# Performance work log

Measured on AMD Instinct MI355X. Metric: run time of the kernel, lower is better.

## Reference

```python
import jax, jax.numpy as jnp
import numpy as np

LAYERS, STACKS, K = 10, 3, 2
DILATIONS = [2 ** i for _ in range(STACKS) for i in range(LAYERS)]  # 30 layers


def conv1d(x, w, b=None, dilation=1):
    # x: [N, C_in, T], w: [C_out, C_in, K] (torch Conv1d layout), VALID padding
    out = jax.lax.conv_general_dilated(
        x, w, window_strides=(1,), padding='VALID',
        rhs_dilation=(dilation,), dimension_numbers=('NCH', 'OIH', 'NCH'))
    if b is not None:
        out = out + b[None, :, None]
    return out


def setup_inputs() -> dict:
    key = jax.random.key(0)
    ks = jax.random.split(key, 12)
    s = 0.1  # weight scale to avoid gate saturation
    return {
        'y': jax.random.normal(ks[0], (16, 1, 16384), dtype=jnp.float32),
        'causal_w': jax.random.normal(ks[1], (32, 1, 1), dtype=jnp.float32) * s,
        'causal_b': jax.random.normal(ks[2], (32,), dtype=jnp.float32) * s,
        'filt_w': jax.random.normal(ks[3], (30, 32, 32, K), dtype=jnp.float32) * s,
        'gate_w': jax.random.normal(ks[4], (30, 32, 32, K), dtype=jnp.float32) * s,
        'res_w': jax.random.normal(ks[5], (30, 32, 32, 1), dtype=jnp.float32) * s,
        'skip_w': jax.random.normal(ks[6], (30, 256, 32, 1), dtype=jnp.float32) * s,
        'end1_w': jax.random.normal(ks[7], (256, 256, 1), dtype=jnp.float32) * s,
        'end1_b': jax.random.normal(ks[8], (256,), dtype=jnp.float32) * s,
        'end2_w': jax.random.normal(ks[9], (256, 256, 1), dtype=jnp.float32) * s,
        'end2_b': jax.random.normal(ks[10], (256,), dtype=jnp.float32) * s,
    }


def reference(y, causal_w, causal_b, filt_w, gate_w, res_w, skip_w,
              end1_w, end1_b, end2_w, end2_b):
    x = conv1d(y, causal_w, causal_b)  # [B, 32, T]
    skip = None
    for i, d in enumerate(DILATIONS):
        r = x
        f = jnp.tanh(conv1d(x, filt_w[i], dilation=d))      # [B,32,T-d]
        g = jax.nn.sigmoid(conv1d(x, gate_w[i], dilation=d))
        x = f * g
        s = conv1d(x, skip_w[i])                             # [B,256,T-d]
        t = s.shape[-1]
        skip = s if skip is None else s + skip[:, :, -t:]
        x = conv1d(x, res_w[i])
        x = x + r[:, :, -x.shape[-1]:]
    x = jax.nn.relu(skip)
    x = jax.nn.relu(conv1d(x, end1_w, end1_b))
    x = conv1d(x, end2_w, end2_b)
    return x
```

## Files before the change

kernel.cpp:

```cpp
#include <hip/hip_runtime.h>
#include <hip/hip_bf16.h>
#include <cstdint>

#define NB 16
#define NC 32
#define T0 16384
#define NL 30
#define SKC 256
#define TF 13315
#define WGRP 192
#define XBC 320
#define XBS 20

typedef _Float16 f16;
typedef _Float16 f16x2 __attribute__((ext_vector_type(2)));
typedef _Float16 f16x8 __attribute__((ext_vector_type(8)));
typedef float f32x4 __attribute__((ext_vector_type(4)));
typedef uint32_t u32;

#define MFMA16(a,b,c) __builtin_amdgcn_mfma_f32_16x16x32_f16(a,b,c,0,0,0)

#define SCF (-2.88539008f)
#define SCG (-1.44269504f)
#define CLF 86.6f
#define CLG 43.3f

__device__ __forceinline__ float frcp(float x){
#if __has_builtin(__builtin_amdgcn_rcpf)
  return __builtin_amdgcn_rcpf(x);
#else
  return 1.f/x;
#endif
}
__device__ __forceinline__ float fexp2(float x){
#if __has_builtin(__builtin_amdgcn_exp2f)
  return __builtin_amdgcn_exp2f(x);
#else
  return exp2f(x);
#endif
}
__device__ __forceinline__ float clampf(float x, float c){
#if __has_builtin(__builtin_amdgcn_fmed3f)
  return __builtin_amdgcn_fmed3f(x, -c, c);
#else
  return fminf(fmaxf(x, -c), c);
#endif
}
__device__ __forceinline__ u32 pk2(float x, float y){
#if __has_builtin(__builtin_amdgcn_cvt_pkrtz)
  return __builtin_bit_cast(u32, __builtin_amdgcn_cvt_pkrtz(x, y));
#else
  f16x2 r; r.x = (f16)x; r.y = (f16)y;
  return __builtin_bit_cast(u32, r);
#endif
}
__device__ __forceinline__ u32 pkadd(u32 a, u32 b){
  f16x2 s = __builtin_bit_cast(f16x2, a) + __builtin_bit_cast(f16x2, b);
  return __builtin_bit_cast(u32, s);
}
__device__ __forceinline__ size_t zfrag_off(int lz, int q){
  return (size_t)(lz & ~63)*NC + (size_t)(((lz>>4)&3)*512 + (q*16 + (lz&15))*8);
}
__device__ __forceinline__ int sigma_co(int q, int j){
  return (j < 4) ? (4*q + j) : (12 + 4*q + j);
}

__global__ __launch_bounds__(256) void prep3(
    const float* __restrict__ sw, const float* __restrict__ e1w,
    const float* __restrict__ e2w, const float* __restrict__ fw,
    const float* __restrict__ gw, const float* __restrict__ rw,
    f16* __restrict__ wsk, f16* __restrict__ e1f, f16* __restrict__ e2f,
    f16* __restrict__ fgpf, f16* __restrict__ ggpf, u32* __restrict__ rwp){
  int idx = blockIdx.x*256 + threadIdx.x;
  if (idx < 30720){
    int lane = idx & 63, mt = (idx>>6)&15, i = idx>>10;
    int m = mt*16 + (lane&15);
    int q = lane >> 4;
    const float* s = sw + ((size_t)i*SKC + m)*NC;
    f16* dp = wsk + (size_t)idx*8;
    #pragma unroll
    for (int j=0;j<8;j++) dp[j] = (f16)s[sigma_co(q, j)];
  } else if (idx < 38912){
    int j2 = idx - 30720;
    int lane = j2&63, mt = (j2>>6)&15, ks = j2>>10;
    int m = mt*16 + (lane&15);
    int k = ks*32 + (lane>>4)*8;
    const float* s = e1w + (size_t)m*SKC + k;
    f16* dp = e1f + (size_t)j2*8;
    #pragma unroll
    for (int j=0;j<8;j++) dp[j] = (f16)s[j];
  } else if (idx < 47104){
    int j2 = idx - 38912;
    int lane = j2&63, mt = (j2>>6)&15, ks = j2>>10;
    int m = mt*16 + (lane&15);
    int k = ks*32 + (lane>>4)*8;
    const float* s = e2w + (size_t)m*SKC + k;
    f16* dp = e2f + (size_t)j2*8;
    #pragma unroll
    for (int j=0;j<8;j++) dp[j] = (f16)s[j];
  } else if (idx < 77824){
    int j2 = idx - 47104;
    const float* s = fw + (size_t)j2*2;
    size_t base = (size_t)(j2 >> 5) * 64;
    int ci = j2 & 31;
    fgpf[base + ci]      = (f16)(s[0]*SCF);
    fgpf[base + 32 + ci] = (f16)(s[1]*SCF);
  } else if (idx < 108544){
    int j2 = idx - 77824;
    const float* s = gw + (size_t)j2*2;
    size_t base = (size_t)(j2 >> 5) * 64;
    int ci = j2 & 31;
    ggpf[base + ci]      = (f16)(s[0]*SCG);
    ggpf[base + 32 + ci] = (f16)(s[1]*SCG);
  } else if (idx < 123904){
    int j2 = idx - 108544;
    int i = j2 >> 9, c = (j2>>4)&31, pj = j2&15;
    const float* s = rw + ((size_t)i*NC + c)*NC;
    int q = pj >> 2, j0 = (2*pj) & 7;
    int c0 = sigma_co(q, j0);
    f16x2 p; p.x = (f16)s[c0]; p.y = (f16)s[c0+1];
    rwp[j2] = __builtin_bit_cast(u32, p);
  }
}

struct LW { f16x8 af[4]; f16x8 ag[4]; f16x8 ar[2]; };
__device__ __forceinline__ void lw_load(LW& w, const f16* __restrict__ fp,
    const f16* __restrict__ gp, const u32* __restrict__ rp, int lane){
  int m = lane & 15, q8 = (lane >> 4) * 8, q4 = (lane >> 4) * 4;
  #pragma unroll
  for (int mh = 0; mh < 2; mh++){
    #pragma unroll
    for (int tap = 0; tap < 2; tap++){
      w.af[mh*2+tap] = *(const f16x8*)&fp[((mh*16+m)*2+tap)*32 + q8];
      w.ag[mh*2+tap] = *(const f16x8*)&gp[((mh*16+m)*2+tap)*32 + q8];
    }
    w.ar[mh] = *(const f16x8*)&rp[(mh*16+m)*16 + q4];
  }
}

__device__ __forceinline__ void tile_core(const LW& w,
    uint4 a, uint4 b, uint2 rb0, uint2 rb1,
    uint4& zfrag, uint2& xo0, uint2& xo1){
  f16x8 A  = __builtin_bit_cast(f16x8, a);
  f16x8 Bt = __builtin_bit_cast(f16x8, b);
  f32x4 z4 = {0.f,0.f,0.f,0.f};
  f32x4 fa0 = MFMA16(w.af[0], A, z4); fa0 = MFMA16(w.af[1], Bt, fa0);
  f32x4 fa1 = MFMA16(w.af[2], A, z4); fa1 = MFMA16(w.af[3], Bt, fa1);
  f32x4 ga0 = MFMA16(w.ag[0], A, z4); ga0 = MFMA16(w.ag[1], Bt, ga0);
  f32x4 ga1 = MFMA16(w.ag[2], A, z4); ga1 = MFMA16(w.ag[3], Bt, ga1);
  u32 zq[4];
  #pragma unroll
  for (int mh = 0; mh < 2; mh++){
    f32x4 fv = mh ? fa1 : fa0;
    f32x4 gv = mh ? ga1 : ga0;
    float zz[4];
    #pragma unroll
    for (int r = 0; r < 4; r++){
      float t = fexp2(clampf(fv[r], CLF));
      float u = fexp2(clampf(gv[r], CLG));
      zz[r] = (1.f - t) * frcp((1.f + t) * (1.f + u));
    }
    zq[mh*2+0] = pk2(zz[0], zz[1]);
    zq[mh*2+1] = pk2(zz[2], zz[3]);
  }
  zfrag = make_uint4(zq[0], zq[1], zq[2], zq[3]);
  f16x8 zB = __builtin_bit_cast(f16x8, zfrag);
  f32x4 r0 = MFMA16(w.ar[0], zB, z4);
  f32x4 r1 = MFMA16(w.ar[1], zB, z4);
  xo0.x = pkadd(pk2(r0[0], r0[1]), rb0.x);
  xo0.y = pkadd(pk2(r0[2], r0[3]), rb0.y);
  xo1.x = pkadd(pk2(r1[0], r1[1]), rb1.x);
  xo1.y = pkadd(pk2(r1[2], r1[3]), rb1.y);
}

struct Trim7 { int t[7]; };

__global__ __launch_bounds__(256, 3) void group7m(
    const f16* __restrict__ xin, const float* __restrict__ y,
    const float* __restrict__ cw, const float* __restrict__ cb, int tc0,
    f16* __restrict__ xout, f16* __restrict__ zbase, int g0,
    int Lfinal, int TcAct, int zrows, int xpb,
    const f16* __restrict__ fgpf, const f16* __restrict__ ggpf,
    const u32* __restrict__ rwp, Trim7 trims){
  __shared__ u32 xb[2][XBC*XBS];
  int tid = threadIdx.x, b = blockIdx.y, o0 = blockIdx.x*WGRP;
  int lane = tid & 63, widx = tid >> 6;
  int Cf = Lfinal - o0; if (Cf > WGRP) Cf = WGRP;
  int Cin = Cf + 127;
  for (int p = tid; p < Cin; p += 256){
    u32* dst = &xb[0][p*XBS];
    if (y != nullptr){
      float yv = y[(size_t)b*T0 + tc0 + o0 + p];
      #pragma unroll
      for (int j = 0; j < 16; j++)
        dst[j] = pk2(fmaf(cw[2*j], yv, cb[2*j]), fmaf(cw[2*j+1], yv, cb[2*j+1]));
    } else {
      const uint4* src = (const uint4*)(xin + ((size_t)b*xpb + o0 + p)*NC);
      uint4* d4 = (uint4*)dst;
      d4[0]=src[0]; d4[1]=src[1]; d4[2]=src[2]; d4[3]=src[3];
    }
  }
  __syncthreads();
  int cur = 0;
  int tl = lane & 15, q = lane >> 4;
  size_t zlayer = (size_t)512*zrows;
  LW w;
  lw_load(w, fgpf + (size_t)g0*2048, ggpf + (size_t)g0*2048,
          rwp + (size_t)g0*512, lane);
  #pragma unroll 1
  for (int li = 0; li < 7; li++){
    int d = 1 << li;
    int count = Cf + 128 - (2 << li);
    LW wn;
    if (li < 6)
      lw_load(wn, fgpf + (size_t)(g0+li+1)*2048, ggpf + (size_t)(g0+li+1)*2048,
              rwp + (size_t)(g0+li+1)*512, lane);
    f16* zl = zbase + (size_t)(g0+li)*zlayer + (size_t)b*zrows*NC;
    int trim = trims.t[li];
    int ntiles = (count + 15) >> 4;
    for (int ti = widx; ti < ntiles; ti += 4){
      int c = ti*16 + tl;
      const u32* xc = &xb[cur][c*XBS];
      const u32* xd = &xb[cur][(c+d)*XBS];
      uint4 a  = *(const uint4*)&xc[q*4];
      uint4 b4 = *(const uint4*)&xd[q*4];
      uint2 rb0 = *(const uint2*)&xd[q*2];
      uint2 rb1 = *(const uint2*)&xd[8 + q*2];
      uint4 zf; uint2 xo0, xo1;
      tile_core(w, a, b4, rb0, rb1, zf, xo0, xo1);
      u32* xn = &xb[cur^1][c*XBS];
      *(uint2*)&xn[q*2] = xo0;
      *(uint2*)&xn[8 + q*2] = xo1;
      int lz = o0 + c - trim;
      if (c < count && lz >= 0 && lz < TcAct)
        *(uint4*)(zl + zfrag_off(lz, q)) = zf;
    }
    __syncthreads();
    if (li < 6) w = wn;
    cur ^= 1;
  }
  for (int p = tid; p < Cf; p += 256){
    const uint4* s4 = (const uint4*)&xb[cur][p*XBS];
    uint4* dd = (uint4*)(xout + ((size_t)b*xpb + o0 + p)*NC);
    dd[0]=s4[0]; dd[1]=s4[1]; dd[2]=s4[2]; dd[3]=s4[3];
  }
}

__global__ __launch_bounds__(256, 3) void singlem(
    const f16* __restrict__ xin, f16* __restrict__ xout, f16* __restrict__ zl,
    const f16* __restrict__ fp, const f16* __restrict__ gp,
    const u32* __restrict__ rp, int Tout, int d, int trim, int TcAct,
    int zrows, int xpb){
  int tid = threadIdx.x, b = blockIdx.y;
  int lane = tid & 63, widx = tid >> 6;
  int t0A = (blockIdx.x*8 + widx*2) * 16;
  if (t0A >= Tout) return;
  int haveB = (t0A + 16) < Tout;
  LW w;
  lw_load(w, fp, gp, rp, lane);
  int tl = lane & 15, q = lane >> 4;
  const f16* xbase = xin + (size_t)b*xpb*NC;
  int cA = t0A + tl;
  const f16* xcA = xbase + (size_t)cA*NC;
  const f16* xdA = xcA + (size_t)d*NC;
  uint4 aA  = *(const uint4*)(xcA + q*8);
  uint4 bA  = *(const uint4*)(xdA + q*8);
  uint2 r0A = *(const uint2*)(xdA + q*4);
  uint2 r1A = *(const uint2*)(xdA + 16 + q*4);
  int cB = cA + 16;
  const f16* xcB = xbase + (size_t)cB*NC;
  const f16* xdB = xcB + (size_t)d*NC;
  uint4 aB  = *(const uint4*)(xcB + q*8);
  uint4 bB  = *(const uint4*)(xdB + q*8);
  uint2 r0B = *(const uint2*)(xdB + q*4);
  uint2 r1B = *(const uint2*)(xdB + 16 + q*4);

  uint4 zfA, zfB; uint2 xo0A, xo1A, xo0B, xo1B;
  tile_core(w, aA, bA, r0A, r1A, zfA, xo0A, xo1A);
  tile_core(w, aB, bB, r0B, r1B, zfB, xo0B, xo1B);

  if (cA < Tout){
    f16* xoc = xout + ((size_t)b*xpb + cA)*NC;
    *(uint2*)(xoc + q*4) = xo0A;
    *(uint2*)(xoc + 16 + q*4) = xo1A;
  }
  if (haveB && cB < Tout){
    f16* xoc = xout + ((size_t)b*xpb + cB)*NC;
    *(uint2*)(xoc + q*4) = xo0B;
    *(uint2*)(xoc + 16 + q*4) = xo1B;
  }
  f16* zlb = zl + (size_t)b*zrows*NC;
  {
    int lz = cA - trim;
    if (cA < Tout && lz >= 0 && lz < TcAct)
      *(uint4*)(zlb + zfrag_off(lz, q)) = zfA;
  }
  if (haveB){
    int lz = cB - trim;
    if (cB < Tout && lz >= 0 && lz < TcAct)
      *(uint4*)(zlb + zfrag_off(lz, q)) = zfB;
  }
}

__global__ __launch_bounds__(256, 3) void skipend(
    const f16* __restrict__ zbase,
    const f16* __restrict__ wsk, const f16* __restrict__ e1f,
    const float* __restrict__ e1b, const f16* __restrict__ e2f,
    const float* __restrict__ e2b, float* __restrict__ out,
    int tc0, int TcAct, int zrows){
  __shared__ u32 smem[64*132];
  int tid = threadIdx.x, b = blockIdx.y, t0 = blockIdx.x*64;
  int w = tid>>6, lane = tid&63;
  int tl = lane & 15;
  int q  = lane >> 4;
  const uint4* wsk4 = (const uint4*)wsk;
  const uint4* e1f4 = (const uint4*)e1f;
  const uint4* e2f4 = (const uint4*)e2f;
  const uint4* zp = (const uint4*)(zbase + ((size_t)b*zrows + t0)*NC) + lane;
  size_t zstep4 = (size_t)64*zrows;

  f32x4 acc[4][4];
  #pragma unroll
  for (int j=0;j<4;j++)
    #pragma unroll
    for (int tt=0;tt<4;tt++) acc[j][tt] = f32x4{0.f,0.f,0.f,0.f};

  uint4 zA[4], aA[4], zB[4], aB[4];
  #pragma unroll
  for (int tt=0;tt<4;tt++) zA[tt] = zp[tt*64];
  #pragma unroll
  for (int j=0;j<4;j++) aA[j] = wsk4[(size_t)(w*4+j)*64 + lane];

  #pragma unroll 1
  for (int l = 0; l < NL; l += 2){
    #pragma unroll
    for (int tt=0;tt<4;tt++) zB[tt] = zp[(size_t)(l+1)*zstep4 + tt*64];
    #pragma unroll
    for (int j=0;j<4;j++)
      aB[j] = wsk4[(size_t)(l+1)*1024 + (w*4+j)*64 + lane];
    #pragma unroll
    for (int j=0;j<4;j++){
      f16x8 a = __builtin_bit_cast(f16x8, aA[j]);
      #pragma unroll
      for (int tt=0;tt<4;tt++)
        acc[j][tt] = MFMA16(a, __builtin_bit_cast(f16x8, zA[tt]), acc[j][tt]);
    }
    if (l+2 < NL){
      #pragma unroll
      for (int tt=0;tt<4;tt++) zA[tt] = zp[(size_t)(l+2)*zstep4 + tt*64];
      #pragma unroll
      for (int j=0;j<4;j++)
        aA[j] = wsk4[(size_t)(l+2)*1024 + (w*4+j)*64 + lane];
    }
    #pragma unroll
    for (int j=0;j<4;j++){
      f16x8 a = __builtin_bit_cast(f16x8, aB[j]);
      #pragma unroll
      for (int tt=0;tt<4;tt++)
        acc[j][tt] = MFMA16(a, __builtin_bit_cast(f16x8, zB[tt]), acc[j][tt]);
    }
  }
  int rq = q*4;
  #pragma unroll
  for (int j=0;j<4;j++){
    int c0 = (w*4+j)*16 + rq;
    #pragma unroll
    for (int tt=0;tt<4;tt++){
      int t = tt*16 + tl;
      u32 p0 = pk2(fmaxf(acc[j][tt][0],0.f), fmaxf(acc[j][tt][1],0.f));
      u32 p1 = pk2(fmaxf(acc[j][tt][2],0.f), fmaxf(acc[j][tt][3],0.f));
      *(uint2*)&smem[t*132 + (c0>>1)] = make_uint2(p0, p1);
    }
  }
  __syncthreads();
  #pragma unroll
  for (int j=0;j<4;j++)
    #pragma unroll
    for (int tt=0;tt<4;tt++) acc[j][tt] = f32x4{0.f,0.f,0.f,0.f};
  #pragma unroll
  for (int ks=0;ks<8;ks++){
    f16x8 zb[4];
    #pragma unroll
    for (int tt=0;tt<4;tt++)
      zb[tt] = *(const f16x8*)&smem[(tt*16+tl)*132 + ks*16 + q*4];
    #pragma unroll
    for (int j=0;j<4;j++){
      f16x8 a = __builtin_bit_cast(f16x8, e1f4[(size_t)(ks*16 + w*4+j)*64 + lane]);
      #pragma unroll
      for (int tt=0;tt<4;tt++)
        acc[j][tt] = MFMA16(a, zb[tt], acc[j][tt]);
    }
  }
  __syncthreads();
  #pragma unroll
  for (int j=0;j<4;j++){
    int c0 = (w*4+j)*16 + rq;
    float4 bv = *(const float4*)&e1b[c0];
    #pragma unroll
    for (int tt=0;tt<4;tt++){
      int t = tt*16 + tl;
      u32 p0 = pk2(fmaxf(acc[j][tt][0]+bv.x,0.f), fmaxf(acc[j][tt][1]+bv.y,0.f));
      u32 p1 = pk2(fmaxf(acc[j][tt][2]+bv.z,0.f), fmaxf(acc[j][tt][3]+bv.w,0.f));
      *(uint2*)&smem[t*132 + (c0>>1)] = make_uint2(p0, p1);
    }
  }
  __syncthreads();
  #pragma unroll
  for (int j=0;j<4;j++)
    #pragma unroll
    for (int tt=0;tt<4;tt++) acc[j][tt] = f32x4{0.f,0.f,0.f,0.f};
  #pragma unroll
  for (int ks=0;ks<8;ks++){
    f16x8 zb[4];
    #pragma unroll
    for (int tt=0;tt<4;tt++)
      zb[tt] = *(const f16x8*)&smem[(tt*16+tl)*132 + ks*16 + q*4];
    #pragma unroll
    for (int j=0;j<4;j++){
      f16x8 a = __builtin_bit_cast(f16x8, e2f4[(size_t)(ks*16 + w*4+j)*64 + lane]);
      #pragma unroll
      for (int tt=0;tt<4;tt++)
        acc[j][tt] = MFMA16(a, zb[tt], acc[j][tt]);
    }
  }
  #pragma unroll
  for (int j=0;j<4;j++){
    int c0 = (w*4+j)*16 + rq;
    float4 bv = *(const float4*)&e2b[c0];
    #pragma unroll
    for (int tt=0;tt<4;tt++){
      int t = tt*16 + tl;
      if (t0 + t < TcAct){
        float* op = out + ((size_t)b*SKC + c0)*TF + tc0 + t0 + t;
        op[0*TF] = acc[j][tt][0] + bv.x;
        op[1*TF] = acc[j][tt][1] + bv.y;
        op[2*TF] = acc[j][tt][2] + bv.z;
        op[3*TF] = acc[j][tt][3] + bv.w;
      }
    }
  }
}

extern "C" void kernel_launch(void* const* d_in, const int* in_sizes, int n_in,
                              void* d_out, int out_size, void* d_ws, size_t ws_size,
                              hipStream_t stream) {
  (void)in_sizes; (void)n_in; (void)out_size;
  const float* y   = (const float*)d_in[0];
  const float* cw  = (const float*)d_in[1];
  const float* cb  = (const float*)d_in[2];
  const float* fw  = (const float*)d_in[3];
  const float* gw  = (const float*)d_in[4];
  const float* rw  = (const float*)d_in[5];
  const float* sw  = (const float*)d_in[6];
  const float* e1w = (const float*)d_in[7];
  const float* e1b = (const float*)d_in[8];
  const float* e2w = (const float*)d_in[9];
  const float* e2b = (const float*)d_in[10];
  float* out = (float*)d_out;
  char* ws = (char*)d_ws;

  const size_t fixedW = 1060864;
  int TCc = 0, xpb = 0;
  for (int c = 1; c <= 6; c++){
    int tcc = (((TF + c - 1)/c) + 63) & ~63;
    int xp  = tcc + 3264;
    size_t need = fixedW + 2*(size_t)xp*1024 + (size_t)NL*512*(size_t)tcc*2;
    if (need <= ws_size){ TCc = tcc; xpb = xp; break; }
  }
  if (!TCc){ TCc = 2240; xpb = 2240 + 3264; }

  f16* wsk   = (f16*)(ws);
  f16* e1f   = (f16*)(ws +   491520);
  f16* e2f   = (f16*)(ws +   622592);
  f16* fgpf  = (f16*)(ws +  753664);
  f16* ggpf  = (f16*)(ws +  876544);
  u32* rwp   = (u32*)(ws +  999424);
  f16* xpA   = (f16*)(ws + fixedW);
  f16* xpB   = (f16*)(ws + fixedW + (size_t)xpb*1024);
  f16* zstack = (f16*)(ws + fixedW + 2*(size_t)xpb*1024);

  int S[NL+1]; S[NL] = 0;
  for (int i = NL-1; i >= 0; i--) S[i] = S[i+1] + (1 << (i % 10));

  prep3<<<dim3(484), 256, 0, stream>>>(sw, e1w, e2w, fw, gw, rw,
                                       wsk, e1f, e2f, fgpf, ggpf, rwp);

  f16* bufs[2] = {xpA, xpB};
  for (int tc0 = 0; tc0 < TF; tc0 += TCc){
    int TcAct = TF - tc0; if (TcAct > TCc) TcAct = TCc;
    int cur = 0;
    for (int s = 0; s < 3; s++){
      int g0 = s*10;
      Trim7 tr;
      for (int li = 0; li < 7; li++) tr.t[li] = S[g0+li+1];
      int Lfinal = TcAct + S[g0+7];
      const f16* gin = (s == 0) ? (const f16*)nullptr : bufs[cur];
      const float* yArg = (s == 0) ? y : (const float*)nullptr;
      int nxt = (s == 0) ? 0 : (cur ^ 1);
      group7m<<<dim3((Lfinal + WGRP-1)/WGRP, NB), 256, 0, stream>>>(
          gin, yArg, cw, cb, tc0, bufs[nxt], zstack, g0, Lfinal, TcAct,
          TCc, xpb, fgpf, ggpf, rwp, tr);
      cur = nxt;
      for (int i = g0+7; i <= g0+9; i++){
        int d = 1 << (i % 10);
        int Tout = TcAct + S[i+1];
        singlem<<<dim3((Tout + 127)/128, NB), 256, 0, stream>>>(
            bufs[cur], bufs[cur^1], zstack + (size_t)i*512*TCc,
            fgpf + (size_t)i*2048, ggpf + (size_t)i*2048, rwp + (size_t)i*512,
            Tout, d, S[i+1], TcAct, TCc, xpb);
        cur ^= 1;
      }
    }
    skipend<<<dim3((TcAct + 63)/64, NB), 256, 0, stream>>>(
        zstack, wsk, e1f, e1b, e2f, e2b, out, tc0, TcAct, TCc);
  }
}
```

Before: 698.3 us.

## Stage skip-layer z tiles through a double-buffered LDS ring in skipend

Before, each of the four waves in a skipend block loaded the same z tiles from global memory. Now the block loads each z tile cooperatively once, with every thread fetching one uint4, and stages three layers at a time in a double-buffered LDS ring. The next group's global loads are held in registers and overlap the current group's MFMAs. Skip weights are now loaded just before use with no prefetch, and each group adds a block barrier. The occupancy hint rises from 3 to 4 blocks per SIMD, which caps registers further and may cause spills.

```diff
diff --git a/kernel.cpp b/kernel.cpp
--- a/kernel.cpp
+++ b/kernel.cpp
@@ -302,7 +302,7 @@
   }
 }
 
-__global__ __launch_bounds__(256, 3) void skipend(
+__global__ __launch_bounds__(256, 4) void skipend(
     const f16* __restrict__ zbase,
     const f16* __restrict__ wsk, const f16* __restrict__ e1f,
     const float* __restrict__ e1b, const f16* __restrict__ e2f,
@@ -316,7 +316,7 @@
   const uint4* wsk4 = (const uint4*)wsk;
   const uint4* e1f4 = (const uint4*)e1f;
   const uint4* e2f4 = (const uint4*)e2f;
-  const uint4* zp = (const uint4*)(zbase + ((size_t)b*zrows + t0)*NC) + lane;
+  const uint4* zsrc = (const uint4*)(zbase + ((size_t)b*zrows + t0)*NC) + tid;
   size_t zstep4 = (size_t)64*zrows;
 
   f32x4 acc[4][4];
@@ -325,41 +325,59 @@
     #pragma unroll
     for (int tt=0;tt<4;tt++) acc[j][tt] = f32x4{0.f,0.f,0.f,0.f};
 
-  uint4 zA[4], aA[4], zB[4], aB[4];
-  #pragma unroll
-  for (int tt=0;tt<4;tt++) zA[tt] = zp[tt*64];
-  #pragma unroll
-  for (int j=0;j<4;j++) aA[j] = wsk4[(size_t)(w*4+j)*64 + lane];
+  uint4* ring = (uint4*)smem;
+  uint4 pz0, pz1, pz2;
+  pz0 = zsrc[0]; pz1 = zsrc[zstep4]; pz2 = zsrc[2*zstep4];
+  ring[tid] = pz0; ring[256 + tid] = pz1; ring[512 + tid] = pz2;
+  pz0 = zsrc[3*zstep4]; pz1 = zsrc[4*zstep4]; pz2 = zsrc[5*zstep4];
+  __syncthreads();
 
   #pragma unroll 1
-  for (int l = 0; l < NL; l += 2){
-    #pragma unroll
-    for (int tt=0;tt<4;tt++) zB[tt] = zp[(size_t)(l+1)*zstep4 + tt*64];
-    #pragma unroll
-    for (int j=0;j<4;j++)
-      aB[j] = wsk4[(size_t)(l+1)*1024 + (w*4+j)*64 + lane];
-    #pragma unroll
-    for (int j=0;j<4;j++){
-      f16x8 a = __builtin_bit_cast(f16x8, aA[j]);
-      #pragma unroll
-      for (int tt=0;tt<4;tt++)
-        acc[j][tt] = MFMA16(a, __builtin_bit_cast(f16x8, zA[tt]), acc[j][tt]);
-    }
-    if (l+2 < NL){
-      #pragma unroll
-      for (int tt=0;tt<4;tt++) zA[tt] = zp[(size_t)(l+2)*zstep4 + tt*64];
-      #pragma unroll
-      for (int j=0;j<4;j++)
-        aA[j] = wsk4[(size_t)(l+2)*1024 + (w*4+j)*64 + lane];
-    }
-    #pragma unroll
-    for (int j=0;j<4;j++){
-      f16x8 a = __builtin_bit_cast(f16x8, aB[j]);
-      #pragma unroll
-      for (int tt=0;tt<4;tt++)
-        acc[j][tt] = MFMA16(a, __builtin_bit_cast(f16x8, zB[tt]), acc[j][tt]);
-    }
-  }
+  for (int g = 0; g < 10; g++){
+    const uint4* zr = (const uint4*)smem + (g&1)*768;
+    int lbase = g*3;
+    #pragma unroll
+    for (int k = 0; k < 3; k++){
+      uint4 aw0 = wsk4[(size_t)(lbase+k)*1024 + (w*4+0)*64 + lane];
+      uint4 aw1 = wsk4[(size_t)(lbase+k)*1024 + (w*4+1)*64 + lane];
+      uint4 aw2 = wsk4[(size_t)(lbase+k)*1024 + (w*4+2)*64 + lane];
+      uint4 aw3 = wsk4[(size_t)(lbase+k)*1024 + (w*4+3)*64 + lane];
+      f16x8 zb0 = *(const f16x8*)&zr[k*256 + 0*64 + lane];
+      f16x8 zb1 = *(const f16x8*)&zr[k*256 + 1*64 + lane];
+      f16x8 zb2 = *(const f16x8*)&zr[k*256 + 2*64 + lane];
+      f16x8 zb3 = *(const f16x8*)&zr[k*256 + 3*64 + lane];
+      f16x8 a0 = __builtin_bit_cast(f16x8, aw0);
+      f16x8 a1 = __builtin_bit_cast(f16x8, aw1);
+      f16x8 a2 = __builtin_bit_cast(f16x8, aw2);
+      f16x8 a3 = __builtin_bit_cast(f16x8, aw3);
+      acc[0][0] = MFMA16(a0, zb0, acc[0][0]);
+      acc[0][1] = MFMA16(a0, zb1, acc[0][1]);
+      acc[0][2] = MFMA16(a0, zb2, acc[0][2]);
+      acc[0][3] = MFMA16(a0, zb3, acc[0][3]);
+      acc[1][0] = MFMA16(a1, zb0, acc[1][0]);
+      acc[1][1] = MFMA16(a1, zb1, acc[1][1]);
+      acc[1][2] = MFMA16(a1, zb2, acc[1][2]);
+      acc[1][3] = MFMA16(a1, zb3, acc[1][3]);
+      acc[2][0] = MFMA16(a2, zb0, acc[2][0]);
+      acc[2][1] = MFMA16(a2, zb1, acc[2][1]);
+      acc[2][2] = MFMA16(a2, zb2, acc[2][2]);
+      acc[2][3] = MFMA16(a2, zb3, acc[2][3]);
+      acc[3][0] = MFMA16(a3, zb0, acc[3][0]);
+      acc[3][1] = MFMA16(a3, zb1, acc[3][1]);
+      acc[3][2] = MFMA16(a3, zb2, acc[3][2]);
+      acc[3][3] = MFMA16(a3, zb3, acc[3][3]);
+    }
+    if (g < 9){
+      uint4* wr = (uint4*)smem + ((g+1)&1)*768;
+      wr[tid] = pz0; wr[256 + tid] = pz1; wr[512 + tid] = pz2;
+      if (g < 8){
+        size_t nb = (size_t)(3*(g+2))*zstep4;
+        pz0 = zsrc[nb]; pz1 = zsrc[nb + zstep4]; pz2 = zsrc[nb + 2*zstep4];
+      }
+      __syncthreads();
+    }
+  }
+  __syncthreads();
   int rq = q*4;
   #pragma unroll
   for (int j=0;j<4;j++){
```

Measured after the change: 717.4 us. 2.7% more time.
